# Kernel optimization log

Measured on AMD Instinct MI355X. Metric: run time of the kernel, lower is better.

Reference implementation:

```python
import jax, jax.numpy as jnp
import numpy as np
from jax import lax


def _binarize(t):
    # sign binarization to +1/-1 (zero maps to -1, matching torch.where(t > 0, 1, -1))
    return jnp.where(t > 0, 1.0, -1.0).astype(t.dtype)


def _bconv(x, w, b):
    # binary conv: binarize input and weights, then standard 3x3 'same' conv
    y = lax.conv_general_dilated(
        _binarize(x), _binarize(w),
        window_strides=(1, 1), padding=((1, 1), (1, 1)),
        dimension_numbers=('NCHW', 'OIHW', 'NCHW'))
    return y + b[None, :, None, None]


def _maxpool2(x):
    return lax.reduce_window(x, -jnp.inf, lax.max, (1, 1, 2, 2), (1, 1, 2, 2), 'VALID')


def setup_inputs() -> dict:
    key = jax.random.key(0)
    ks = jax.random.split(key, 13)
    s = 0.1
    return {
        'x': jax.random.normal(ks[0], (4096, 1, 28, 28), jnp.float32),
        'w1': jax.random.normal(ks[1], (32, 1, 3, 3), jnp.float32) * s,
        'b1': jax.random.normal(ks[2], (32,), jnp.float32) * s,
        'w2': jax.random.normal(ks[3], (64, 32, 3, 3), jnp.float32) * s,
        'b2': jax.random.normal(ks[4], (64,), jnp.float32) * s,
        'w3': jax.random.normal(ks[5], (16, 64, 3, 3), jnp.float32) * s,
        'b3': jax.random.normal(ks[6], (16,), jnp.float32) * s,
        'fc1_w': jax.random.normal(ks[7], (256, 16 * 7 * 7), jnp.float32) * s,
        'fc1_b': jax.random.normal(ks[8], (256,), jnp.float32) * s,
        'fc2_w': jax.random.normal(ks[9], (128, 256), jnp.float32) * s,
        'fc2_b': jax.random.normal(ks[10], (128,), jnp.float32) * s,
        'fc3_w': jax.random.normal(ks[11], (10, 128), jnp.float32) * s,
        'fc3_b': jax.random.normal(ks[12], (10,), jnp.float32) * s,
    }


def reference(x, w1, b1, w2, b2, w3, b3, fc1_w, fc1_b, fc2_w, fc2_b, fc3_w, fc3_b):
    h = jax.nn.relu(_maxpool2(_bconv(x, w1, b1)))      # [B,32,14,14]
    h = jax.nn.relu(_maxpool2(_bconv(h, w2, b2)))      # [B,64,7,7]
    h = jax.nn.relu(_bconv(h, w3, b3))                 # [B,16,7,7]
    h = h.reshape(-1, 16 * 7 * 7)
    h = jax.nn.relu(h @ fc1_w.T + fc1_b)
    h = jax.nn.relu(h @ fc2_w.T + fc2_b)
    return h @ fc3_w.T + fc3_b                          # [B,10]
```

## Files before the change

### kernel.cpp

```cpp
#include <hip/hip_runtime.h>
#include <cstdint>

#define OFF_W1T   4096
#define OFF_W2T   823296
#define OFF_H3T   954368
#define OFF_H1T   14061568
#define OFF_H2T   18255872

#define TW_WB1    0
#define TW_W2     32
#define TW_W3     608
#define TW_CORR2  896
#define TW_CORR3  1920
#define TW_TLE1   2176
#define TW_TGE1   2208
#define TW_TLE2   2240
#define TW_TGE2   2304

__device__ __forceinline__ int imin2(int a, int b) { return a < b ? a : b; }
__device__ __forceinline__ int imax2(int a, int b) { return a > b ? a : b; }

__global__ __launch_bounds__(256) void prep(
    const float* __restrict__ w1, const float* __restrict__ b1,
    const float* __restrict__ w2, const float* __restrict__ b2,
    const float* __restrict__ w3,
    const float* __restrict__ fc1_w, const float* __restrict__ fc2_w,
    int* __restrict__ tab, float* __restrict__ w1T, float* __restrict__ w2T) {
    int t = threadIdx.x;
    uint32_t* utab = (uint32_t*)tab;
    if (blockIdx.x == 0) {
        if (t < 32) {
            uint32_t b = 0;
            for (int k = 0; k < 9; ++k) b |= (w1[t * 9 + k] > 0.f ? 1u : 0u) << k;
            utab[TW_WB1 + t] = b;
            tab[TW_TLE1 + t] = (int)floorf((9.f + b1[t]) * 0.5f);
            tab[TW_TGE1 + t] = (int)floorf(-b1[t]) + 1;
        }
        if (t >= 32 && t < 96) {
            int oc = t - 32;
            tab[TW_TLE2 + oc] = (int)floorf((288.f + b2[oc]) * 0.5f);
            tab[TW_TGE2 + oc] = (int)floorf(-b2[oc]) + 1;
        }
        for (int idx = t; idx < 576; idx += 256) {
            int oc = idx / 9, tap = idx % 9;
            int kh = tap / 3, kw = tap % 3;
            uint32_t b = 0;
            for (int ic = 0; ic < 32; ++ic)
                b |= (w2[((oc * 32 + ic) * 3 + kh) * 3 + kw] > 0.f ? 1u : 0u) << ic;
            utab[TW_W2 + idx] = b;
        }
        for (int idx = t; idx < 288; idx += 256) {
            int oc = idx / 18, rem = idx % 18;
            int tap = rem >> 1, word = rem & 1;
            int kh = tap / 3, kw = tap % 3;
            uint32_t b = 0;
            for (int ic = 0; ic < 32; ++ic)
                b |= (w3[((oc * 64 + ic + 32 * word) * 3 + kh) * 3 + kw] > 0.f ? 1u : 0u) << ic;
            utab[TW_W3 + idx] = b;
        }
        __syncthreads();
        for (int idx = t; idx < 1024; idx += 256) {
            int pat = idx >> 6, oc = idx & 63;
            int s = 0, n = 0;
            for (int tap = 0; tap < 9; ++tap) {
                int kh = tap / 3, kw = tap % 3;
                bool pad = ((pat & 1) && kh == 0) || ((pat & 2) && kh == 2) ||
                           ((pat & 4) && kw == 0) || ((pat & 8) && kw == 2);
                if (pad) { s += __popc(utab[TW_W2 + oc * 9 + tap]); ++n; }
            }
            tab[TW_CORR2 + idx] = 2 * s - 32 * n;
        }
        {
            int idx = t;
            if (idx < 256) {
                int pat = idx >> 4, oc = idx & 15;
                int s = 0, n = 0;
                for (int tap = 0; tap < 9; ++tap) {
                    int kh = tap / 3, kw = tap % 3;
                    bool pad = ((pat & 1) && kh == 0) || ((pat & 2) && kh == 2) ||
                               ((pat & 4) && kw == 0) || ((pat & 8) && kw == 2);
                    if (pad) {
                        s += __popc(utab[TW_W3 + oc * 18 + tap * 2]) +
                             __popc(utab[TW_W3 + oc * 18 + tap * 2 + 1]);
                        ++n;
                    }
                }
                tab[TW_CORR3 + idx] = 2 * s - 64 * n;
            }
        }
    } else {
        int e = (blockIdx.x - 1) * 256 + t;
        if (e < 204800) {
            int k = e >> 8, n = e & 255;
            w1T[e] = (k < 784) ? fc1_w[n * 784 + k] : 0.f;
        } else {
            int e2 = e - 204800;
            int k = e2 >> 7, n = e2 & 127;
            w2T[e2] = fc2_w[n * 256 + k];
        }
    }
}

#define WV_SIZE 456

__global__ __launch_bounds__(256, 6) void conv_stack(
    const float* __restrict__ x,
    const float* __restrict__ b3,
    const int* __restrict__ tab,
    float* __restrict__ h3T) {
    __shared__ uint32_t SH[4 * WV_SIZE];
    const int t = threadIdx.x;
    const int wid = t >> 6, lane = t & 63;
    const int img = blockIdx.x * 4 + wid;
    uint32_t* W = SH + wid * WV_SIZE;
    const uint32_t* utab = (const uint32_t*)tab;

#pragma unroll
    for (int k = 0; k < 8; ++k) {
        int idx = lane + k * 64;
        if (idx < WV_SIZE) W[idx] = 0;
    }

    if (lane < 28) {
        const float* xr = x + img * 784 + lane * 28;
        uint32_t b = 0;
#pragma unroll
        for (int q = 0; q < 7; ++q) {
            float4 v = *(const float4*)(xr + q * 4);
            b |= (v.x > 0.f ? 1u : 0u) << (q * 4 + 0);
            b |= (v.y > 0.f ? 1u : 0u) << (q * 4 + 1);
            b |= (v.z > 0.f ? 1u : 0u) << (q * 4 + 2);
            b |= (v.w > 0.f ? 1u : 0u) << (q * 4 + 3);
        }
        W[1 + lane] = b << 1;
    }
    __syncthreads();

    for (int it = 0; it < 3; ++it) {
        int p = it * 64 + lane;
        bool act = p < 144;
        int pp = act ? p : 0;
        int Pi = 1 + pp / 12, Pj = 1 + pp % 12;
        int i0 = 2 * Pi, j0 = 2 * Pj;
        uint32_t r0 = W[i0], r1 = W[i0 + 1], r2 = W[i0 + 2], r3 = W[i0 + 3];
        uint32_t f0a = (r0 >> j0) & 7, f0b = (r0 >> (j0 + 1)) & 7;
        uint32_t f1a = (r1 >> j0) & 7, f1b = (r1 >> (j0 + 1)) & 7;
        uint32_t f2a = (r2 >> j0) & 7, f2b = (r2 >> (j0 + 1)) & 7;
        uint32_t f3a = (r3 >> j0) & 7, f3b = (r3 >> (j0 + 1)) & 7;
        uint32_t s00 = f0a | (f1a << 3) | (f2a << 6);
        uint32_t s01 = f0b | (f1b << 3) | (f2b << 6);
        uint32_t s10 = f1a | (f2a << 3) | (f3a << 6);
        uint32_t s11 = f1b | (f2b << 3) | (f3b << 6);
        uint32_t word = 0;
#pragma unroll
        for (int oc = 0; oc < 32; ++oc) {
            uint32_t w = utab[TW_WB1 + oc];
            int m0 = __popc(s00 ^ w), m1 = __popc(s01 ^ w);
            int m2 = __popc(s10 ^ w), m3 = __popc(s11 ^ w);
            int mn = imin2(imin2(m0, m1), imin2(m2, m3));
            word |= (mn <= tab[TW_TLE1 + oc] ? 1u : 0u) << oc;
        }
        if (act) W[32 + (Pi + 1) * 16 + (Pj + 1)] = word;
    }
    {
        int p = lane;
        bool act = p < 52;
        int pp = act ? p : 28;
        int Pi, Pj;
        if (pp < 14)      { Pi = 0;  Pj = pp; }
        else if (pp < 28) { Pi = 13; Pj = pp - 14; }
        else if (pp < 40) { Pi = pp - 28 + 1; Pj = 0; }
        else              { Pi = pp - 40 + 1; Pj = 13; }
        int i0 = 2 * Pi, j0 = 2 * Pj;
        uint32_t r0 = W[i0], r1 = W[i0 + 1], r2 = W[i0 + 2], r3 = W[i0 + 3];
        uint32_t f0a = (r0 >> j0) & 7, f0b = (r0 >> (j0 + 1)) & 7;
        uint32_t f1a = (r1 >> j0) & 7, f1b = (r1 >> (j0 + 1)) & 7;
        uint32_t f2a = (r2 >> j0) & 7, f2b = (r2 >> (j0 + 1)) & 7;
        uint32_t f3a = (r3 >> j0) & 7, f3b = (r3 >> (j0 + 1)) & 7;
        uint32_t smp[4];
        smp[0] = f0a | (f1a << 3) | (f2a << 6);
        smp[1] = f0b | (f1b << 3) | (f2b << 6);
        smp[2] = f1a | (f2a << 3) | (f3a << 6);
        smp[3] = f1b | (f2b << 3) | (f3b << 6);
        uint32_t mb[4];
        int pcm[4];
#pragma unroll
        for (int a = 0; a < 2; ++a) {
            int i = 2 * Pi + a;
            uint32_t vre = 0x1FF;
            if (i == 0)  vre &= ~0x007u;
            if (i == 27) vre &= ~0x1C0u;
#pragma unroll
            for (int bb = 0; bb < 2; ++bb) {
                int j = 2 * Pj + bb;
                uint32_t vce = 0x1FF;
                if (j == 0)  vce &= ~0x049u;
                if (j == 27) vce &= ~0x124u;
                mb[a * 2 + bb] = vre & vce;
                pcm[a * 2 + bb] = __popc(vre & vce);
            }
        }
        uint32_t word = 0;
#pragma unroll
        for (int oc = 0; oc < 32; ++oc) {
            uint32_t w = utab[TW_WB1 + oc];
            int best = -1000;
#pragma unroll
            for (int p4 = 0; p4 < 4; ++p4) {
                int v = pcm[p4] - 2 * __popc((smp[p4] ^ w) & mb[p4]);
                best = imax2(best, v);
            }
            word |= (best >= tab[TW_TGE1 + oc] ? 1u : 0u) << oc;
        }
        if (act) W[32 + (Pi + 1) * 16 + (Pj + 1)] = word;
    }
    __syncthreads();

    {
        uint32_t w2r[9];
#pragma unroll
        for (int k = 0; k < 9; ++k) w2r[k] = utab[TW_W2 + lane * 9 + k];
        const int tle2 = tab[TW_TLE2 + lane];
        const int tge2 = tab[TW_TGE2 + lane];
        const uint32_t* H1 = W + 32;
        uint32_t* H2 = W + 288;

        for (int Pi = 1; Pi <= 5; ++Pi) {
            for (int Pj = 1; Pj <= 5; ++Pj) {
                uint32_t c[16];
#pragma unroll
                for (int r = 0; r < 4; ++r) {
                    uint2 lo = *(const uint2*)&H1[(2 * Pi + r) * 16 + 2 * Pj];
                    uint2 hi = *(const uint2*)&H1[(2 * Pi + r) * 16 + 2 * Pj + 2];
                    c[r * 4 + 0] = lo.x; c[r * 4 + 1] = lo.y;
                    c[r * 4 + 2] = hi.x; c[r * 4 + 3] = hi.y;
                }
                int Sv[4];
#pragma unroll
                for (int a = 0; a < 2; ++a)
#pragma unroll
                    for (int bb = 0; bb < 2; ++bb) {
                        int s = 0;
#pragma unroll
                        for (int kh = 0; kh < 3; ++kh)
#pragma unroll
                            for (int kw = 0; kw < 3; ++kw)
                                s += __popc(c[(a + kh) * 4 + (bb + kw)] ^ w2r[kh * 3 + kw]);
                        Sv[a * 2 + bb] = s;
                    }
                int mn = imin2(imin2(Sv[0], Sv[1]), imin2(Sv[2], Sv[3]));
                uint64_t bal = __ballot(mn <= tle2);
                if (lane == 0) {
                    uint2 wv = make_uint2((uint32_t)bal, (uint32_t)(bal >> 32));
                    *(uint2*)&H2[((Pi + 1) * 9 + (Pj + 1)) * 2] = wv;
                }
            }
        }
        for (int bp = 0; bp < 24; ++bp) {
            int Pi, Pj;
            if (bp < 7)       { Pi = 0; Pj = bp; }
            else if (bp < 14) { Pi = 6; Pj = bp - 7; }
            else if (bp < 19) { Pi = bp - 14 + 1; Pj = 0; }
            else              { Pi = bp - 19 + 1; Pj = 6; }
            uint32_t c[16];
#pragma unroll
            for (int r = 0; r < 4; ++r) {
                uint2 lo = *(const uint2*)&H1[(2 * Pi + r) * 16 + 2 * Pj];
                uint2 hi = *(const uint2*)&H1[(2 * Pi + r) * 16 + 2 * Pj + 2];
                c[r * 4 + 0] = lo.x; c[r * 4 + 1] = lo.y;
                c[r * 4 + 2] = hi.x; c[r * 4 + 3] = hi.y;
            }
            int Sv[4];
#pragma unroll
            for (int a = 0; a < 2; ++a)
#pragma unroll
                for (int bb = 0; bb < 2; ++bb) {
                    int s = 0;
#pragma unroll
                    for (int kh = 0; kh < 3; ++kh)
#pragma unroll
                        for (int kw = 0; kw < 3; ++kw)
                            s += __popc(c[(a + kh) * 4 + (bb + kw)] ^ w2r[kh * 3 + kw]);
                    Sv[a * 2 + bb] = s;
                }
            int best = -100000;
#pragma unroll
            for (int a = 0; a < 2; ++a)
#pragma unroll
                for (int bb = 0; bb < 2; ++bb) {
                    int i = 2 * Pi + a, j = 2 * Pj + bb;
                    int pat = (i == 0 ? 1 : 0) | (i == 13 ? 2 : 0) |
                              (j == 0 ? 4 : 0) | (j == 13 ? 8 : 0);
                    int D = 288 - 2 * Sv[a * 2 + bb] + tab[TW_CORR2 + pat * 64 + lane];
                    best = imax2(best, D);
                }
            uint64_t bal = __ballot(best >= tge2);
            if (lane == 0) {
                uint2 wv = make_uint2((uint32_t)bal, (uint32_t)(bal >> 32));
                *(uint2*)&H2[((Pi + 1) * 9 + (Pj + 1)) * 2] = wv;
            }
        }
    }
    __syncthreads();

    {
        const uint32_t* H2 = W + 288;
        int oc = lane & 15, sub = lane >> 4;
        uint32_t w3r[18];
#pragma unroll
        for (int k = 0; k < 18; ++k) w3r[k] = utab[TW_W3 + oc * 18 + k];
        float bias3 = b3[oc];
        for (int g = 0; g < 13; ++g) {
            int pos = g * 4 + sub;
            bool act = pos < 49;
            int pp = act ? pos : 0;
            int Pi = pp / 7, Pj = pp % 7;
            int s = 0;
#pragma unroll
            for (int kh = 0; kh < 3; ++kh)
#pragma unroll
                for (int kw = 0; kw < 3; ++kw) {
                    uint2 hv = *(const uint2*)&H2[((Pi + kh) * 9 + (Pj + kw)) * 2];
                    s += __popc(hv.x ^ w3r[(kh * 3 + kw) * 2]) +
                         __popc(hv.y ^ w3r[(kh * 3 + kw) * 2 + 1]);
                }
            int pat = (Pi == 0 ? 1 : 0) | (Pi == 6 ? 2 : 0) |
                      (Pj == 0 ? 4 : 0) | (Pj == 6 ? 8 : 0);
            int D = 576 - 2 * s + tab[TW_CORR3 + pat * 16 + oc];
            float h = (float)D + bias3;
            h = h > 0.f ? h : 0.f;
            if (act) h3T[(oc * 49 + pp) * 4096 + img] = h;
        }
    }
}

__global__ __launch_bounds__(256) void fc1_gemm(
    const float* __restrict__ aT,
    const float* __restrict__ bT,
    const float* __restrict__ bias,
    float* __restrict__ oT) {
    const int KC = 80, LD = 68;
    __shared__ float As[KC * LD];
    __shared__ float Bs[KC * LD];
    const int t = threadIdx.x;
    const int tx = t & 15, ty = t >> 4;
    const int img0 = blockIdx.x * 64;
    const int n0 = blockIdx.y * 64;
    float acc[4][4] = {{0.f}};

    for (int kc = 0; kc < 800; kc += KC) {
#pragma unroll
        for (int s = 0; s < 5; ++s) {
            int v = t + s * 256;
            int kk = v >> 4, i4 = (v & 15) * 4;
            *(float4*)&As[kk * LD + i4] =
                *(const float4*)&aT[(kc + kk) * 4096 + img0 + i4];
            *(float4*)&Bs[kk * LD + i4] =
                *(const float4*)&bT[(kc + kk) * 256 + n0 + i4];
        }
        __syncthreads();
#pragma unroll 4
        for (int kk = 0; kk < KC; ++kk) {
            float4 a = *(const float4*)&As[kk * LD + ty * 4];
            float4 b = *(const float4*)&Bs[kk * LD + tx * 4];
            acc[0][0] += a.x * b.x; acc[0][1] += a.x * b.y;
            acc[0][2] += a.x * b.z; acc[0][3] += a.x * b.w;
            acc[1][0] += a.y * b.x; acc[1][1] += a.y * b.y;
            acc[1][2] += a.y * b.z; acc[1][3] += a.y * b.w;
            acc[2][0] += a.z * b.x; acc[2][1] += a.z * b.y;
            acc[2][2] += a.z * b.z; acc[2][3] += a.z * b.w;
            acc[3][0] += a.w * b.x; acc[3][1] += a.w * b.y;
            acc[3][2] += a.w * b.z; acc[3][3] += a.w * b.w;
        }
        __syncthreads();
    }
    float4 bb = *(const float4*)&bias[n0 + tx * 4];
    float bv[4] = {bb.x, bb.y, bb.z, bb.w};
#pragma unroll
    for (int jj = 0; jj < 4; ++jj) {
        float4 ov;
        ov.x = acc[0][jj] + bv[jj]; ov.x = ov.x > 0.f ? ov.x : 0.f;
        ov.y = acc[1][jj] + bv[jj]; ov.y = ov.y > 0.f ? ov.y : 0.f;
        ov.z = acc[2][jj] + bv[jj]; ov.z = ov.z > 0.f ? ov.z : 0.f;
        ov.w = acc[3][jj] + bv[jj]; ov.w = ov.w > 0.f ? ov.w : 0.f;
        *(float4*)&oT[(n0 + tx * 4 + jj) * 4096 + img0 + ty * 4] = ov;
    }
}

__global__ __launch_bounds__(256) void fc2_gemm(
    const float* __restrict__ aT,
    const float* __restrict__ bT,
    const float* __restrict__ bias,
    float* __restrict__ oT) {
    const int KC = 64, LDA = 68, LDB = 36;
    __shared__ float As[KC * LDA];
    __shared__ float Bs[KC * LDB];
    const int t = threadIdx.x;
    const int tx = t & 15, ty = t >> 4;
    const int img0 = blockIdx.x * 64;
    const int n0 = blockIdx.y * 32;
    float acc[4][2] = {{0.f}};

    for (int kc = 0; kc < 256; kc += KC) {
#pragma unroll
        for (int s = 0; s < 4; ++s) {
            int v = t + s * 256;
            int kk = v >> 4, i4 = (v & 15) * 4;
            *(float4*)&As[kk * LDA + i4] =
                *(const float4*)&aT[(kc + kk) * 4096 + img0 + i4];
        }
#pragma unroll
        for (int s = 0; s < 2; ++s) {
            int v = t + s * 256;
            int kk = v >> 3, n4 = (v & 7) * 4;
            *(float4*)&Bs[kk * LDB + n4] =
                *(const float4*)&bT[(kc + kk) * 128 + n0 + n4];
        }
        __syncthreads();
#pragma unroll 4
        for (int kk = 0; kk < KC; ++kk) {
            float4 a = *(const float4*)&As[kk * LDA + ty * 4];
            float2 b = *(const float2*)&Bs[kk * LDB + tx * 2];
            acc[0][0] += a.x * b.x; acc[0][1] += a.x * b.y;
            acc[1][0] += a.y * b.x; acc[1][1] += a.y * b.y;
            acc[2][0] += a.z * b.x; acc[2][1] += a.z * b.y;
            acc[3][0] += a.w * b.x; acc[3][1] += a.w * b.y;
        }
        __syncthreads();
    }
#pragma unroll
    for (int j = 0; j < 2; ++j) {
        int n = n0 + tx * 2 + j;
        float bj = bias[n];
        float4 ov;
        ov.x = acc[0][j] + bj; ov.x = ov.x > 0.f ? ov.x : 0.f;
        ov.y = acc[1][j] + bj; ov.y = ov.y > 0.f ? ov.y : 0.f;
        ov.z = acc[2][j] + bj; ov.z = ov.z > 0.f ? ov.z : 0.f;
        ov.w = acc[3][j] + bj; ov.w = ov.w > 0.f ? ov.w : 0.f;
        *(float4*)&oT[n * 4096 + img0 + ty * 4] = ov;
    }
}

__global__ __launch_bounds__(256) void fc3_gemm(
    const float* __restrict__ aT,
    const float* __restrict__ w,
    const float* __restrict__ bias,
    float* __restrict__ out) {
    int id = blockIdx.x * 256 + threadIdx.x;
    int n = id >> 12, img = id & 4095;
    const float* wr = w + n * 128;
    float a0 = 0.f, a1 = 0.f, a2 = 0.f, a3 = 0.f;
#pragma unroll 8
    for (int k = 0; k < 128; k += 4) {
        a0 += aT[(k + 0) * 4096 + img] * wr[k + 0];
        a1 += aT[(k + 1) * 4096 + img] * wr[k + 1];
        a2 += aT[(k + 2) * 4096 + img] * wr[k + 2];
        a3 += aT[(k + 3) * 4096 + img] * wr[k + 3];
    }
    out[img * 10 + n] = (a0 + a1) + (a2 + a3) + bias[n];
}

extern "C" void kernel_launch(void* const* d_in, const int* in_sizes, int n_in,
                              void* d_out, int out_size, void* d_ws, size_t ws_size,
                              hipStream_t stream) {
    const float* x     = (const float*)d_in[0];
    const float* w1    = (const float*)d_in[1];
    const float* b1    = (const float*)d_in[2];
    const float* w2    = (const float*)d_in[3];
    const float* b2    = (const float*)d_in[4];
    const float* w3    = (const float*)d_in[5];
    const float* b3    = (const float*)d_in[6];
    const float* fc1_w = (const float*)d_in[7];
    const float* fc1_b = (const float*)d_in[8];
    const float* fc2_w = (const float*)d_in[9];
    const float* fc2_b = (const float*)d_in[10];
    const float* fc3_w = (const float*)d_in[11];
    const float* fc3_b = (const float*)d_in[12];
    float* out = (float*)d_out;

    const int B = in_sizes[0] / 784;
    char* ws = (char*)d_ws;
    float* w1T = (float*)(ws + OFF_W1T);
    float* w2T = (float*)(ws + OFF_W2T);
    float* h3T = (float*)(ws + OFF_H3T);
    float* h1T = (float*)(ws + OFF_H1T);
    float* h2T = (float*)(ws + OFF_H2T);
    int* tab = (int*)(ws + OFF_H1T);

    hipLaunchKernelGGL(prep, dim3(929), dim3(256), 0, stream,
                       w1, b1, w2, b2, w3, fc1_w, fc2_w, tab, w1T, w2T);
    hipLaunchKernelGGL(conv_stack, dim3(B / 4), dim3(256), 0, stream,
                       x, b3, tab, h3T);
    hipLaunchKernelGGL(fc1_gemm, dim3(B / 64, 4), dim3(256), 0, stream,
                       h3T, w1T, fc1_b, h1T);
    hipLaunchKernelGGL(fc2_gemm, dim3(B / 64, 4), dim3(256), 0, stream,
                       h1T, w2T, fc2_b, h2T);
    hipLaunchKernelGGL(fc3_gemm, dim3(B * 10 / 256), dim3(256), 0, stream,
                       h2T, fc3_w, fc3_b, out);
}
```

Measured before the change: 207.9 us.

## Split each image across two wavefronts in conv stack and widen FC GEMM blocks

The conv stack now assigns two wavefronts per image instead of one, splitting the input binarization, conv1, conv2 and conv3 positions between them. The interior/border split in conv2 is unified into a single position loop using correction tables. Those correction tables are staged in shared memory per block, and the launch-bounds occupancy hint is raised. The FC1/FC2 GEMMs move to 512-thread blocks with fewer outputs per thread, trading per-thread register reuse for more parallel threads.

New measurement: 218.9 us. +5.3%, slower.

```diff
diff --git a/kernel.cpp b/kernel.cpp
--- a/kernel.cpp
+++ b/kernel.cpp
@@ -101,28 +101,28 @@
     }
 }
 
-#define WV_SIZE 456
-
-__global__ __launch_bounds__(256, 6) void conv_stack(
+#define WV 456
+
+__global__ __launch_bounds__(256, 8) void conv_stack(
     const float* __restrict__ x,
     const float* __restrict__ b3,
     const int* __restrict__ tab,
     float* __restrict__ h3T) {
-    __shared__ uint32_t SH[4 * WV_SIZE];
+    __shared__ int SH[1280 + 2 * WV];
     const int t = threadIdx.x;
     const int wid = t >> 6, lane = t & 63;
-    const int img = blockIdx.x * 4 + wid;
-    uint32_t* W = SH + wid * WV_SIZE;
+    const int iml = wid >> 1, sw = wid & 1;
+    const int img = blockIdx.x * 2 + iml;
     const uint32_t* utab = (const uint32_t*)tab;
-
-#pragma unroll
-    for (int k = 0; k < 8; ++k) {
-        int idx = lane + k * 64;
-        if (idx < WV_SIZE) W[idx] = 0;
-    }
-
-    if (lane < 28) {
-        const float* xr = x + img * 784 + lane * 28;
+    uint32_t* W = (uint32_t*)&SH[1280 + iml * WV];
+
+    for (int i = t; i < 1280; i += 256) SH[i] = tab[TW_CORR2 + i];
+    for (int i = t; i < 2 * WV; i += 256) SH[1280 + i] = 0;
+    __syncthreads();
+
+    if (lane < 14) {
+        int r = sw * 14 + lane;
+        const float* xr = x + img * 784 + r * 28;
         uint32_t b = 0;
 #pragma unroll
         for (int q = 0; q < 7; ++q) {
@@ -132,15 +132,12 @@
             b |= (v.z > 0.f ? 1u : 0u) << (q * 4 + 2);
             b |= (v.w > 0.f ? 1u : 0u) << (q * 4 + 3);
         }
-        W[1 + lane] = b << 1;
+        W[1 + r] = b << 1;
     }
     __syncthreads();
 
-    for (int it = 0; it < 3; ++it) {
-        int p = it * 64 + lane;
-        bool act = p < 144;
-        int pp = act ? p : 0;
-        int Pi = 1 + pp / 12, Pj = 1 + pp % 12;
+    auto conv1_int = [&](int p) {
+        int Pi = 1 + p / 12, Pj = 1 + p % 12;
         int i0 = 2 * Pi, j0 = 2 * Pj;
         uint32_t r0 = W[i0], r1 = W[i0 + 1], r2 = W[i0 + 2], r3 = W[i0 + 3];
         uint32_t f0a = (r0 >> j0) & 7, f0b = (r0 >> (j0 + 1)) & 7;
@@ -160,9 +157,13 @@
             int mn = imin2(imin2(m0, m1), imin2(m2, m3));
             word |= (mn <= tab[TW_TLE1 + oc] ? 1u : 0u) << oc;
         }
-        if (act) W[32 + (Pi + 1) * 16 + (Pj + 1)] = word;
-    }
-    {
+        W[32 + (Pi + 1) * 16 + (Pj + 1)] = word;
+    };
+    if (sw == 0) {
+        conv1_int(lane);
+        conv1_int(64 + lane);
+    } else {
+        if (lane < 16) conv1_int(128 + lane);
         int p = lane;
         bool act = p < 52;
         int pp = act ? p : 28;
@@ -220,48 +221,12 @@
         uint32_t w2r[9];
 #pragma unroll
         for (int k = 0; k < 9; ++k) w2r[k] = utab[TW_W2 + lane * 9 + k];
-        const int tle2 = tab[TW_TLE2 + lane];
         const int tge2 = tab[TW_TGE2 + lane];
         const uint32_t* H1 = W + 32;
         uint32_t* H2 = W + 288;
-
-        for (int Pi = 1; Pi <= 5; ++Pi) {
-            for (int Pj = 1; Pj <= 5; ++Pj) {
-                uint32_t c[16];
-#pragma unroll
-                for (int r = 0; r < 4; ++r) {
-                    uint2 lo = *(const uint2*)&H1[(2 * Pi + r) * 16 + 2 * Pj];
-                    uint2 hi = *(const uint2*)&H1[(2 * Pi + r) * 16 + 2 * Pj + 2];
-                    c[r * 4 + 0] = lo.x; c[r * 4 + 1] = lo.y;
-                    c[r * 4 + 2] = hi.x; c[r * 4 + 3] = hi.y;
-                }
-                int Sv[4];
-#pragma unroll
-                for (int a = 0; a < 2; ++a)
-#pragma unroll
-                    for (int bb = 0; bb < 2; ++bb) {
-                        int s = 0;
-#pragma unroll
-                        for (int kh = 0; kh < 3; ++kh)
-#pragma unroll
-                            for (int kw = 0; kw < 3; ++kw)
-                                s += __popc(c[(a + kh) * 4 + (bb + kw)] ^ w2r[kh * 3 + kw]);
-                        Sv[a * 2 + bb] = s;
-                    }
-                int mn = imin2(imin2(Sv[0], Sv[1]), imin2(Sv[2], Sv[3]));
-                uint64_t bal = __ballot(mn <= tle2);
-                if (lane == 0) {
-                    uint2 wv = make_uint2((uint32_t)bal, (uint32_t)(bal >> 32));
-                    *(uint2*)&H2[((Pi + 1) * 9 + (Pj + 1)) * 2] = wv;
-                }
-            }
-        }
-        for (int bp = 0; bp < 24; ++bp) {
-            int Pi, Pj;
-            if (bp < 7)       { Pi = 0; Pj = bp; }
-            else if (bp < 14) { Pi = 6; Pj = bp - 7; }
-            else if (bp < 19) { Pi = bp - 14 + 1; Pj = 0; }
-            else              { Pi = bp - 19 + 1; Pj = 6; }
+        const int pbeg = sw ? 25 : 0, pend = sw ? 49 : 25;
+        for (int pos = pbeg; pos < pend; ++pos) {
+            int Pi = pos / 7, Pj = pos - Pi * 7;
             uint32_t c[16];
 #pragma unroll
             for (int r = 0; r < 4; ++r) {
@@ -270,7 +235,7 @@
                 c[r * 4 + 0] = lo.x; c[r * 4 + 1] = lo.y;
                 c[r * 4 + 2] = hi.x; c[r * 4 + 3] = hi.y;
             }
-            int Sv[4];
+            int best = -100000;
 #pragma unroll
             for (int a = 0; a < 2; ++a)
 #pragma unroll
@@ -281,17 +246,10 @@
 #pragma unroll
                         for (int kw = 0; kw < 3; ++kw)
                             s += __popc(c[(a + kh) * 4 + (bb + kw)] ^ w2r[kh * 3 + kw]);
-                    Sv[a * 2 + bb] = s;
-                }
-            int best = -100000;
-#pragma unroll
-            for (int a = 0; a < 2; ++a)
-#pragma unroll
-                for (int bb = 0; bb < 2; ++bb) {
                     int i = 2 * Pi + a, j = 2 * Pj + bb;
                     int pat = (i == 0 ? 1 : 0) | (i == 13 ? 2 : 0) |
                               (j == 0 ? 4 : 0) | (j == 13 ? 8 : 0);
-                    int D = 288 - 2 * Sv[a * 2 + bb] + tab[TW_CORR2 + pat * 64 + lane];
+                    int D = 288 - 2 * s + SH[pat * 64 + lane];
                     best = imax2(best, D);
                 }
             uint64_t bal = __ballot(best >= tge2);
@@ -304,13 +262,14 @@
     __syncthreads();
 
     {
-        const uint32_t* H2 = W + 288;
+        const uint32_t* H2 = (const uint32_t*)W + 288;
         int oc = lane & 15, sub = lane >> 4;
         uint32_t w3r[18];
 #pragma unroll
         for (int k = 0; k < 18; ++k) w3r[k] = utab[TW_W3 + oc * 18 + k];
         float bias3 = b3[oc];
-        for (int g = 0; g < 13; ++g) {
+        const int gbeg = sw ? 6 : 0, gend = sw ? 13 : 6;
+        for (int g = gbeg; g < gend; ++g) {
             int pos = g * 4 + sub;
             bool act = pos < 49;
             int pp = act ? pos : 0;
@@ -326,7 +285,7 @@
                 }
             int pat = (Pi == 0 ? 1 : 0) | (Pi == 6 ? 2 : 0) |
                       (Pj == 0 ? 4 : 0) | (Pj == 6 ? 8 : 0);
-            int D = 576 - 2 * s + tab[TW_CORR3 + pat * 16 + oc];
+            int D = 576 - 2 * s + SH[1024 + pat * 16 + oc];
             float h = (float)D + bias3;
             h = h > 0.f ? h : 0.f;
             if (act) h3T[(oc * 49 + pp) * 4096 + img] = h;
@@ -334,7 +293,7 @@
     }
 }
 
-__global__ __launch_bounds__(256) void fc1_gemm(
+__global__ __launch_bounds__(512) void fc1_gemm(
     const float* __restrict__ aT,
     const float* __restrict__ bT,
     const float* __restrict__ bias,
@@ -346,31 +305,32 @@
     const int tx = t & 15, ty = t >> 4;
     const int img0 = blockIdx.x * 64;
     const int n0 = blockIdx.y * 64;
-    float acc[4][4] = {{0.f}};
+    float acc[2][4] = {{0.f}};
 
     for (int kc = 0; kc < 800; kc += KC) {
 #pragma unroll
         for (int s = 0; s < 5; ++s) {
-            int v = t + s * 256;
-            int kk = v >> 4, i4 = (v & 15) * 4;
-            *(float4*)&As[kk * LD + i4] =
-                *(const float4*)&aT[(kc + kk) * 4096 + img0 + i4];
-            *(float4*)&Bs[kk * LD + i4] =
-                *(const float4*)&bT[(kc + kk) * 256 + n0 + i4];
+            int v = t + s * 512;
+            if (v < 1280) {
+                int kk = v >> 4, i4 = (v & 15) * 4;
+                *(float4*)&As[kk * LD + i4] =
+                    *(const float4*)&aT[(kc + kk) * 4096 + img0 + i4];
+            } else {
+                int v2 = v - 1280;
+                int kk = v2 >> 4, i4 = (v2 & 15) * 4;
+                *(float4*)&Bs[kk * LD + i4] =
+                    *(const float4*)&bT[(kc + kk) * 256 + n0 + i4];
+            }
         }
         __syncthreads();
 #pragma unroll 4
         for (int kk = 0; kk < KC; ++kk) {
-            float4 a = *(const float4*)&As[kk * LD + ty * 4];
+            float2 a = *(const float2*)&As[kk * LD + ty * 2];
             float4 b = *(const float4*)&Bs[kk * LD + tx * 4];
             acc[0][0] += a.x * b.x; acc[0][1] += a.x * b.y;
             acc[0][2] += a.x * b.z; acc[0][3] += a.x * b.w;
             acc[1][0] += a.y * b.x; acc[1][1] += a.y * b.y;
             acc[1][2] += a.y * b.z; acc[1][3] += a.y * b.w;
-            acc[2][0] += a.z * b.x; acc[2][1] += a.z * b.y;
-            acc[2][2] += a.z * b.z; acc[2][3] += a.z * b.w;
-            acc[3][0] += a.w * b.x; acc[3][1] += a.w * b.y;
-            acc[3][2] += a.w * b.z; acc[3][3] += a.w * b.w;
         }
         __syncthreads();
     }
@@ -378,16 +338,14 @@
     float bv[4] = {bb.x, bb.y, bb.z, bb.w};
 #pragma unroll
     for (int jj = 0; jj < 4; ++jj) {
-        float4 ov;
+        float2 ov;
         ov.x = acc[0][jj] + bv[jj]; ov.x = ov.x > 0.f ? ov.x : 0.f;
         ov.y = acc[1][jj] + bv[jj]; ov.y = ov.y > 0.f ? ov.y : 0.f;
-        ov.z = acc[2][jj] + bv[jj]; ov.z = ov.z > 0.f ? ov.z : 0.f;
-        ov.w = acc[3][jj] + bv[jj]; ov.w = ov.w > 0.f ? ov.w : 0.f;
-        *(float4*)&oT[(n0 + tx * 4 + jj) * 4096 + img0 + ty * 4] = ov;
-    }
-}
-
-__global__ __launch_bounds__(256) void fc2_gemm(
+        *(float2*)&oT[(n0 + tx * 4 + jj) * 4096 + img0 + ty * 2] = ov;
+    }
+}
+
+__global__ __launch_bounds__(512) void fc2_gemm(
     const float* __restrict__ aT,
     const float* __restrict__ bT,
     const float* __restrict__ bias,
@@ -399,19 +357,18 @@
     const int tx = t & 15, ty = t >> 4;
     const int img0 = blockIdx.x * 64;
     const int n0 = blockIdx.y * 32;
-    float acc[4][2] = {{0.f}};
+    float acc[2][2] = {{0.f}};
 
     for (int kc = 0; kc < 256; kc += KC) {
 #pragma unroll
-        for (int s = 0; s < 4; ++s) {
-            int v = t + s * 256;
+        for (int s = 0; s < 2; ++s) {
+            int v = t + s * 512;
             int kk = v >> 4, i4 = (v & 15) * 4;
             *(float4*)&As[kk * LDA + i4] =
                 *(const float4*)&aT[(kc + kk) * 4096 + img0 + i4];
         }
-#pragma unroll
-        for (int s = 0; s < 2; ++s) {
-            int v = t + s * 256;
+        {
+            int v = t;
             int kk = v >> 3, n4 = (v & 7) * 4;
             *(float4*)&Bs[kk * LDB + n4] =
                 *(const float4*)&bT[(kc + kk) * 128 + n0 + n4];
@@ -419,12 +376,10 @@
         __syncthreads();
 #pragma unroll 4
         for (int kk = 0; kk < KC; ++kk) {
-            float4 a = *(const float4*)&As[kk * LDA + ty * 4];
+            float2 a = *(const float2*)&As[kk * LDA + ty * 2];
             float2 b = *(const float2*)&Bs[kk * LDB + tx * 2];
             acc[0][0] += a.x * b.x; acc[0][1] += a.x * b.y;
             acc[1][0] += a.y * b.x; acc[1][1] += a.y * b.y;
-            acc[2][0] += a.z * b.x; acc[2][1] += a.z * b.y;
-            acc[3][0] += a.w * b.x; acc[3][1] += a.w * b.y;
         }
         __syncthreads();
     }
@@ -432,12 +387,10 @@
     for (int j = 0; j < 2; ++j) {
         int n = n0 + tx * 2 + j;
         float bj = bias[n];
-        float4 ov;
+        float2 ov;
         ov.x = acc[0][j] + bj; ov.x = ov.x > 0.f ? ov.x : 0.f;
         ov.y = acc[1][j] + bj; ov.y = ov.y > 0.f ? ov.y : 0.f;
-        ov.z = acc[2][j] + bj; ov.z = ov.z > 0.f ? ov.z : 0.f;
-        ov.w = acc[3][j] + bj; ov.w = ov.w > 0.f ? ov.w : 0.f;
-        *(float4*)&oT[n * 4096 + img0 + ty * 4] = ov;
+        *(float2*)&oT[n * 4096 + img0 + ty * 2] = ov;
     }
 }
 
@@ -489,11 +442,11 @@
 
     hipLaunchKernelGGL(prep, dim3(929), dim3(256), 0, stream,
                        w1, b1, w2, b2, w3, fc1_w, fc2_w, tab, w1T, w2T);
-    hipLaunchKernelGGL(conv_stack, dim3(B / 4), dim3(256), 0, stream,
+    hipLaunchKernelGGL(conv_stack, dim3(B / 2), dim3(256), 0, stream,
                        x, b3, tab, h3T);
-    hipLaunchKernelGGL(fc1_gemm, dim3(B / 64, 4), dim3(256), 0, stream,
+    hipLaunchKernelGGL(fc1_gemm, dim3(B / 64, 4), dim3(512), 0, stream,
                        h3T, w1T, fc1_b, h1T);
-    hipLaunchKernelGGL(fc2_gemm, dim3(B / 64, 4), dim3(256), 0, stream,
+    hipLaunchKernelGGL(fc2_gemm, dim3(B / 64, 4), dim3(512), 0, stream,
                        h1T, w2T, fc2_b, h2T);
     hipLaunchKernelGGL(fc3_gemm, dim3(B * 10 / 256), dim3(256), 0, stream,
                        h2T, fc3_w, fc3_b, out);
```

## Split conv stack across two waves per image and double-buffer FC GEMMs

Applied to the files above, without the earlier changes.

The conv_stack kernel now uses 512 threads per block, so two wavefronts share each image. They divide the conv1, conv2 and conv3 position work between them, and the conv2/conv3 correction tables are cached in LDS instead of being read from global memory. fc1 and fc2 now stage tiles into double-buffered LDS through global_load_lds, which lets the next chunk's loads overlap the current chunk's FMAs. The trade-offs are more LDS per block, extra barriers, and reliance on correct wait/barrier semantics for the async LDS loads.

New measurement: 218.4 us. 1.05x slower.

```diff
diff --git a/kernel.cpp b/kernel.cpp
--- a/kernel.cpp
+++ b/kernel.cpp
@@ -19,6 +19,16 @@
 
 __device__ __forceinline__ int imin2(int a, int b) { return a < b ? a : b; }
 __device__ __forceinline__ int imax2(int a, int b) { return a > b ? a : b; }
+
+__device__ __forceinline__ void gload16(const float* g, float* lbase, int lane) {
+#if __has_builtin(__builtin_amdgcn_global_load_lds)
+    __builtin_amdgcn_global_load_lds(
+        (const __attribute__((address_space(1))) uint32_t*)g,
+        (__attribute__((address_space(3))) uint32_t*)lbase, 16, 0, 0);
+#else
+    *(float4*)&lbase[lane * 4] = *(const float4*)g;
+#endif
+}
 
 __global__ __launch_bounds__(256) void prep(
     const float* __restrict__ w1, const float* __restrict__ b1,
@@ -101,28 +111,28 @@
     }
 }
 
-#define WV_SIZE 456
-
-__global__ __launch_bounds__(256, 6) void conv_stack(
+#define WV 456
+
+__global__ __launch_bounds__(512, 8) void conv_stack(
     const float* __restrict__ x,
     const float* __restrict__ b3,
     const int* __restrict__ tab,
     float* __restrict__ h3T) {
-    __shared__ uint32_t SH[4 * WV_SIZE];
+    __shared__ int SH[1280 + 4 * WV];
     const int t = threadIdx.x;
     const int wid = t >> 6, lane = t & 63;
-    const int img = blockIdx.x * 4 + wid;
-    uint32_t* W = SH + wid * WV_SIZE;
+    const int iml = wid >> 1, sw = wid & 1;
+    const int img = blockIdx.x * 4 + iml;
     const uint32_t* utab = (const uint32_t*)tab;
-
-#pragma unroll
-    for (int k = 0; k < 8; ++k) {
-        int idx = lane + k * 64;
-        if (idx < WV_SIZE) W[idx] = 0;
-    }
-
-    if (lane < 28) {
-        const float* xr = x + img * 784 + lane * 28;
+    uint32_t* W = (uint32_t*)&SH[1280 + iml * WV];
+
+    for (int i = t; i < 1280; i += 512) SH[i] = tab[TW_CORR2 + i];
+    for (int i = t; i < 4 * WV; i += 512) SH[1280 + i] = 0;
+    __syncthreads();
+
+    if (lane < 14) {
+        int r = sw * 14 + lane;
+        const float* xr = x + img * 784 + r * 28;
         uint32_t b = 0;
 #pragma unroll
         for (int q = 0; q < 7; ++q) {
@@ -132,15 +142,12 @@
             b |= (v.z > 0.f ? 1u : 0u) << (q * 4 + 2);
             b |= (v.w > 0.f ? 1u : 0u) << (q * 4 + 3);
         }
-        W[1 + lane] = b << 1;
+        W[1 + r] = b << 1;
     }
     __syncthreads();
 
-    for (int it = 0; it < 3; ++it) {
-        int p = it * 64 + lane;
-        bool act = p < 144;
-        int pp = act ? p : 0;
-        int Pi = 1 + pp / 12, Pj = 1 + pp % 12;
+    auto conv1_int = [&](int p) {
+        int Pi = 1 + p / 12, Pj = 1 + p % 12;
         int i0 = 2 * Pi, j0 = 2 * Pj;
         uint32_t r0 = W[i0], r1 = W[i0 + 1], r2 = W[i0 + 2], r3 = W[i0 + 3];
         uint32_t f0a = (r0 >> j0) & 7, f0b = (r0 >> (j0 + 1)) & 7;
@@ -160,9 +167,13 @@
             int mn = imin2(imin2(m0, m1), imin2(m2, m3));
             word |= (mn <= tab[TW_TLE1 + oc] ? 1u : 0u) << oc;
         }
-        if (act) W[32 + (Pi + 1) * 16 + (Pj + 1)] = word;
-    }
-    {
+        W[32 + (Pi + 1) * 16 + (Pj + 1)] = word;
+    };
+    if (sw == 0) {
+        conv1_int(lane);
+        conv1_int(64 + lane);
+    } else {
+        if (lane < 16) conv1_int(128 + lane);
         int p = lane;
         bool act = p < 52;
         int pp = act ? p : 28;
@@ -225,38 +236,36 @@
         const uint32_t* H1 = W + 32;
         uint32_t* H2 = W + 288;
 
-        for (int Pi = 1; Pi <= 5; ++Pi) {
-            for (int Pj = 1; Pj <= 5; ++Pj) {
-                uint32_t c[16];
-#pragma unroll
-                for (int r = 0; r < 4; ++r) {
-                    uint2 lo = *(const uint2*)&H1[(2 * Pi + r) * 16 + 2 * Pj];
-                    uint2 hi = *(const uint2*)&H1[(2 * Pi + r) * 16 + 2 * Pj + 2];
-                    c[r * 4 + 0] = lo.x; c[r * 4 + 1] = lo.y;
-                    c[r * 4 + 2] = hi.x; c[r * 4 + 3] = hi.y;
+        for (int q = sw; q < 25; q += 2) {
+            int Pi = 1 + q / 5, Pj = 1 + q % 5;
+            uint32_t c[16];
+#pragma unroll
+            for (int r = 0; r < 4; ++r) {
+                uint2 lo = *(const uint2*)&H1[(2 * Pi + r) * 16 + 2 * Pj];
+                uint2 hi = *(const uint2*)&H1[(2 * Pi + r) * 16 + 2 * Pj + 2];
+                c[r * 4 + 0] = lo.x; c[r * 4 + 1] = lo.y;
+                c[r * 4 + 2] = hi.x; c[r * 4 + 3] = hi.y;
+            }
+            int mn = 100000;
+#pragma unroll
+            for (int a = 0; a < 2; ++a)
+#pragma unroll
+                for (int bb = 0; bb < 2; ++bb) {
+                    int s = 0;
+#pragma unroll
+                    for (int kh = 0; kh < 3; ++kh)
+#pragma unroll
+                        for (int kw = 0; kw < 3; ++kw)
+                            s += __popc(c[(a + kh) * 4 + (bb + kw)] ^ w2r[kh * 3 + kw]);
+                    mn = imin2(mn, s);
                 }
-                int Sv[4];
-#pragma unroll
-                for (int a = 0; a < 2; ++a)
-#pragma unroll
-                    for (int bb = 0; bb < 2; ++bb) {
-                        int s = 0;
-#pragma unroll
-                        for (int kh = 0; kh < 3; ++kh)
-#pragma unroll
-                            for (int kw = 0; kw < 3; ++kw)
-                                s += __popc(c[(a + kh) * 4 + (bb + kw)] ^ w2r[kh * 3 + kw]);
-                        Sv[a * 2 + bb] = s;
-                    }
-                int mn = imin2(imin2(Sv[0], Sv[1]), imin2(Sv[2], Sv[3]));
-                uint64_t bal = __ballot(mn <= tle2);
-                if (lane == 0) {
-                    uint2 wv = make_uint2((uint32_t)bal, (uint32_t)(bal >> 32));
-                    *(uint2*)&H2[((Pi + 1) * 9 + (Pj + 1)) * 2] = wv;
-                }
-            }
-        }
-        for (int bp = 0; bp < 24; ++bp) {
+            uint64_t bal = __ballot(mn <= tle2);
+            if (lane == 0) {
+                uint2 wv = make_uint2((uint32_t)bal, (uint32_t)(bal >> 32));
+                *(uint2*)&H2[((Pi + 1) * 9 + (Pj + 1)) * 2] = wv;
+            }
+        }
+        for (int bp = sw; bp < 24; bp += 2) {
             int Pi, Pj;
             if (bp < 7)       { Pi = 0; Pj = bp; }
             else if (bp < 14) { Pi = 6; Pj = bp - 7; }
@@ -270,7 +279,7 @@
                 c[r * 4 + 0] = lo.x; c[r * 4 + 1] = lo.y;
                 c[r * 4 + 2] = hi.x; c[r * 4 + 3] = hi.y;
             }
-            int Sv[4];
+            int best = -100000;
 #pragma unroll
             for (int a = 0; a < 2; ++a)
 #pragma unroll
@@ -281,17 +290,10 @@
 #pragma unroll
                         for (int kw = 0; kw < 3; ++kw)
                             s += __popc(c[(a + kh) * 4 + (bb + kw)] ^ w2r[kh * 3 + kw]);
-                    Sv[a * 2 + bb] = s;
-                }
-            int best = -100000;
-#pragma unroll
-            for (int a = 0; a < 2; ++a)
-#pragma unroll
-                for (int bb = 0; bb < 2; ++bb) {
                     int i = 2 * Pi + a, j = 2 * Pj + bb;
                     int pat = (i == 0 ? 1 : 0) | (i == 13 ? 2 : 0) |
                               (j == 0 ? 4 : 0) | (j == 13 ? 8 : 0);
-                    int D = 288 - 2 * Sv[a * 2 + bb] + tab[TW_CORR2 + pat * 64 + lane];
+                    int D = 288 - 2 * s + SH[pat * 64 + lane];
                     best = imax2(best, D);
                 }
             uint64_t bal = __ballot(best >= tge2);
@@ -304,13 +306,14 @@
     __syncthreads();
 
     {
-        const uint32_t* H2 = W + 288;
+        const uint32_t* H2 = (const uint32_t*)W + 288;
         int oc = lane & 15, sub = lane >> 4;
         uint32_t w3r[18];
 #pragma unroll
         for (int k = 0; k < 18; ++k) w3r[k] = utab[TW_W3 + oc * 18 + k];
         float bias3 = b3[oc];
-        for (int g = 0; g < 13; ++g) {
+        const int gbeg = sw ? 6 : 0, gend = sw ? 13 : 6;
+        for (int g = gbeg; g < gend; ++g) {
             int pos = g * 4 + sub;
             bool act = pos < 49;
             int pp = act ? pos : 0;
@@ -326,7 +329,7 @@
                 }
             int pat = (Pi == 0 ? 1 : 0) | (Pi == 6 ? 2 : 0) |
                       (Pj == 0 ? 4 : 0) | (Pj == 6 ? 8 : 0);
-            int D = 576 - 2 * s + tab[TW_CORR3 + pat * 16 + oc];
+            int D = 576 - 2 * s + SH[1024 + pat * 16 + oc];
             float h = (float)D + bias3;
             h = h > 0.f ? h : 0.f;
             if (act) h3T[(oc * 49 + pp) * 4096 + img] = h;
@@ -339,30 +342,39 @@
     const float* __restrict__ bT,
     const float* __restrict__ bias,
     float* __restrict__ oT) {
-    const int KC = 80, LD = 68;
-    __shared__ float As[KC * LD];
-    __shared__ float Bs[KC * LD];
+    const int KC = 40;
+    __shared__ float As[2][KC * 64];
+    __shared__ float Bs[2][KC * 64];
     const int t = threadIdx.x;
+    const int lane = t & 63, wid = t >> 6;
     const int tx = t & 15, ty = t >> 4;
     const int img0 = blockIdx.x * 64;
     const int n0 = blockIdx.y * 64;
     float acc[4][4] = {{0.f}};
 
-    for (int kc = 0; kc < 800; kc += KC) {
-#pragma unroll
-        for (int s = 0; s < 5; ++s) {
-            int v = t + s * 256;
-            int kk = v >> 4, i4 = (v & 15) * 4;
-            *(float4*)&As[kk * LD + i4] =
-                *(const float4*)&aT[(kc + kk) * 4096 + img0 + i4];
-            *(float4*)&Bs[kk * LD + i4] =
-                *(const float4*)&bT[(kc + kk) * 256 + n0 + i4];
-        }
-        __syncthreads();
-#pragma unroll 4
+    auto stage = [&](int buf, int kc) {
+        for (int s = wid; s < 20; s += 4) {
+            int seg = s < 10 ? s : s - 10;
+            int kk = seg * 4 + (lane >> 4);
+            int c = (lane & 15) * 4;
+            if (s < 10)
+                gload16(&aT[(kc + kk) * 4096 + img0 + c], &As[buf][seg * 256], lane);
+            else
+                gload16(&bT[(kc + kk) * 256 + n0 + c], &Bs[buf][seg * 256], lane);
+        }
+    };
+
+    stage(0, 0);
+    __syncthreads();
+    for (int ch = 0; ch < 20; ++ch) {
+        int buf = ch & 1;
+        if (ch + 1 < 20) stage(buf ^ 1, (ch + 1) * KC);
+        const float* A = As[buf];
+        const float* B = Bs[buf];
+#pragma unroll 8
         for (int kk = 0; kk < KC; ++kk) {
-            float4 a = *(const float4*)&As[kk * LD + ty * 4];
-            float4 b = *(const float4*)&Bs[kk * LD + tx * 4];
+            float4 a = *(const float4*)&A[kk * 64 + ty * 4];
+            float4 b = *(const float4*)&B[kk * 64 + tx * 4];
             acc[0][0] += a.x * b.x; acc[0][1] += a.x * b.y;
             acc[0][2] += a.x * b.z; acc[0][3] += a.x * b.w;
             acc[1][0] += a.y * b.x; acc[1][1] += a.y * b.y;
@@ -392,35 +404,42 @@
     const float* __restrict__ bT,
     const float* __restrict__ bias,
     float* __restrict__ oT) {
-    const int KC = 64, LDA = 68, LDB = 36;
-    __shared__ float As[KC * LDA];
-    __shared__ float Bs[KC * LDB];
+    const int KC = 64;
+    __shared__ float As[2][KC * 64];
+    __shared__ float Bs[2][KC * 32];
     const int t = threadIdx.x;
+    const int lane = t & 63, wid = t >> 6;
     const int tx = t & 15, ty = t >> 4;
     const int img0 = blockIdx.x * 64;
     const int n0 = blockIdx.y * 32;
     float acc[4][2] = {{0.f}};
 
-    for (int kc = 0; kc < 256; kc += KC) {
-#pragma unroll
-        for (int s = 0; s < 4; ++s) {
-            int v = t + s * 256;
-            int kk = v >> 4, i4 = (v & 15) * 4;
-            *(float4*)&As[kk * LDA + i4] =
-                *(const float4*)&aT[(kc + kk) * 4096 + img0 + i4];
-        }
-#pragma unroll
-        for (int s = 0; s < 2; ++s) {
-            int v = t + s * 256;
-            int kk = v >> 3, n4 = (v & 7) * 4;
-            *(float4*)&Bs[kk * LDB + n4] =
-                *(const float4*)&bT[(kc + kk) * 128 + n0 + n4];
-        }
-        __syncthreads();
-#pragma unroll 4
+    auto stage = [&](int buf, int kc) {
+        for (int s = wid; s < 24; s += 4) {
+            if (s < 16) {
+                int kk = s * 4 + (lane >> 4);
+                int c = (lane & 15) * 4;
+                gload16(&aT[(kc + kk) * 4096 + img0 + c], &As[buf][s * 256], lane);
+            } else {
+                int seg = s - 16;
+                int kk = seg * 8 + (lane >> 3);
+                int c = (lane & 7) * 4;
+                gload16(&bT[(kc + kk) * 128 + n0 + c], &Bs[buf][seg * 256], lane);
+            }
+        }
+    };
+
+    stage(0, 0);
+    __syncthreads();
+    for (int ch = 0; ch < 4; ++ch) {
+        int buf = ch & 1;
+        if (ch + 1 < 4) stage(buf ^ 1, (ch + 1) * KC);
+        const float* A = As[buf];
+        const float* B = Bs[buf];
+#pragma unroll 8
         for (int kk = 0; kk < KC; ++kk) {
-            float4 a = *(const float4*)&As[kk * LDA + ty * 4];
-            float2 b = *(const float2*)&Bs[kk * LDB + tx * 2];
+            float4 a = *(const float4*)&A[kk * 64 + ty * 4];
+            float2 b = *(const float2*)&B[kk * 32 + tx * 2];
             acc[0][0] += a.x * b.x; acc[0][1] += a.x * b.y;
             acc[1][0] += a.y * b.x; acc[1][1] += a.y * b.y;
             acc[2][0] += a.z * b.x; acc[2][1] += a.z * b.y;
@@ -489,7 +508,7 @@
 
     hipLaunchKernelGGL(prep, dim3(929), dim3(256), 0, stream,
                        w1, b1, w2, b2, w3, fc1_w, fc2_w, tab, w1T, w2T);
-    hipLaunchKernelGGL(conv_stack, dim3(B / 4), dim3(256), 0, stream,
+    hipLaunchKernelGGL(conv_stack, dim3(B / 4), dim3(512), 0, stream,
                        x, b3, tab, h3T);
     hipLaunchKernelGGL(fc1_gemm, dim3(B / 64, 4), dim3(256), 0, stream,
                        h3T, w1T, fc1_b, h1T);
```
